# Performance work log

Hardware: AMD Instinct MI355X
Metric: run time of the kernel (lower is better)

The kernel has to match this reference:

```python
import jax, jax.numpy as jnp
import numpy as np
from jax import lax

NX, NY = 6, 6
NB = NX * NY            # 36 blocks
B, S = 64, 256          # batch, sample_count
EPS = 1e-6

def build_edges(nx, ny):
    edges = []
    for i in range(nx):
        for j in range(ny):
            for dx, dy in [(-1, 0), (0, -1), (0, 1), (1, 0)]:
                x, y = i + dx, j + dy
                if 0 <= x < nx and 0 <= y < ny:
                    edges.append((j * nx + i, y * nx + x))
    return np.array(edges, np.int32)   # (120, 2)

EDGES_NP = build_edges(NX, NY)
NE = len(EDGES_NP)  # 120

def setup_inputs() -> dict:
    key = jax.random.key(0)
    ks = jax.random.split(key, 24)
    f32 = jnp.float32
    d = {
        "image":      jax.random.normal(ks[0], (B, 1, 32, 32), f32),
        "edge_noise": jax.random.uniform(ks[1], (B, S, NE), f32),
        "u_s":        jax.random.uniform(ks[2], (B, S, NB), f32),
        "u_d":        jax.random.uniform(ks[3], (B, S, NB), f32),
        # CNN params (OIHW)
        "cw1": jax.random.normal(ks[4], (32, 1, 5, 5), f32) * 0.05,
        "cb1": jnp.zeros((32,), f32),
        "cw2": jax.random.normal(ks[5], (32, 32, 5, 5), f32) * 0.05,
        "cb2": jnp.zeros((32,), f32),
        "cw3": jax.random.normal(ks[6], (64, 32, 5, 5), f32) * 0.05,
        "cb3": jnp.zeros((64,), f32),
        "cw4": jax.random.normal(ks[7], (64, 64, 5, 5), f32) * 0.05,
        "cb4": jnp.zeros((64,), f32),
        # is_connected MLP
        "wc1": jax.random.normal(ks[8], (256, 256), f32) * 0.05,
        "bc1": jnp.zeros((256,), f32),
        "wc2": jax.random.normal(ks[9], (256, NE), f32) * 0.05,
        "bc2": jnp.zeros((NE,), f32),
        # is_endpoint MLP
        "we1": jax.random.normal(ks[10], (256, 256), f32) * 0.05,
        "be1": jnp.zeros((256,), f32),
        "we2": jax.random.normal(ks[11], (256, NB), f32) * 0.05,
        "be2": jnp.zeros((NB,), f32),
        "edges": jnp.asarray(EDGES_NP),  # (NE, 2) int32, constants
    }
    return d

def _conv(x, w, b):
    y = lax.conv_general_dilated(x, w, (1, 1), 'VALID',
                                 dimension_numbers=('NCHW', 'OIHW', 'NCHW'))
    return y + b[None, :, None, None]

def _pool2(x):
    return lax.reduce_window(x, -jnp.inf, lax.max, (1, 1, 2, 2), (1, 1, 2, 2), 'VALID')

def reference(image, edge_noise, u_s, u_d,
              cw1, cb1, cw2, cb2, cw3, cb3, cw4, cb4,
              wc1, bc1, wc2, bc2, we1, be1, we2, be2, edges):
    # ---- CNN feature extractor ----
    h = _conv(image, cw1, cb1)
    h = _conv(h, cw2, cb2)
    h = _pool2(h)
    h = _conv(h, cw3, cb3)
    h = _conv(h, cw4, cb4)
    h = _pool2(h)
    emb = h.reshape(h.shape[0], -1)              # (B, 256)

    # ---- heads ----
    p_conn = jax.nn.sigmoid(jax.nn.relu(emb @ wc1 + bc1) @ wc2 + bc2)   # (B, NE)
    p_ep   = jax.nn.sigmoid(jax.nn.relu(emb @ we1 + be1) @ we2 + be2)   # (B, NB)

    pc = jnp.clip(p_conn, EPS, 1.0 - EPS)
    pe = jnp.clip(p_ep, EPS, 1.0 - EPS)
    cat = pe / pe.sum(-1, keepdims=True)
    logcat = jnp.log(cat)                        # (B, NB)

    # ---- Monte-Carlo sampling (ISED blackbox) ----
    conn = (edge_noise < pc[:, None, :]).astype(pc.dtype)               # (B,S,NE) Bernoulli
    g_s = -jnp.log(-jnp.log(jnp.clip(u_s, EPS, 1.0 - EPS)))
    g_d = -jnp.log(-jnp.log(jnp.clip(u_d, EPS, 1.0 - EPS)))
    s_idx = jnp.argmax(logcat[:, None, :] + g_s, axis=-1)               # (B,S) categorical
    d_idx = jnp.argmax(logcat[:, None, :] + g_d, axis=-1)               # (B,S)

    # ---- batched BFS reachability via boolean matrix squaring ----
    oh_u = jax.nn.one_hot(edges[:, 0], NB, dtype=pc.dtype)              # (NE, NB)
    oh_v = jax.nn.one_hot(edges[:, 1], NB, dtype=pc.dtype)
    e_sym = jnp.einsum('eu,ev->euv', oh_u, oh_v) + jnp.einsum('eu,ev->evu', oh_u, oh_v)
    A = jnp.minimum(jnp.einsum('bse,euv->bsuv', conn, e_sym), 1.0)      # (B,S,36,36)

    R = jnp.minimum(A + jnp.eye(NB, dtype=A.dtype), 1.0)
    for _ in range(6):                           # (I+A)^(2^6), covers path len<=36
        R = jnp.minimum(R @ R, 1.0)
    P = jnp.minimum(A @ R, 1.0)                  # paths of length >= 1 (BFS semantics)

    Pv = jnp.take_along_axis(P, s_idx[:, :, None, None], axis=2)[:, :, 0, :]  # (B,S,36)
    exists = (jnp.take_along_axis(Pv, d_idx[:, :, None], axis=2)[:, :, 0] > 0.5).astype(pc.dtype)  # (B,S)

    # ---- sample-probability weighting (differentiable ISED estimator) ----
    logw = (conn * jnp.log(pc)[:, None, :] + (1.0 - conn) * jnp.log1p(-pc)[:, None, :]).sum(-1)
    logw = logw + jnp.take_along_axis(logcat, s_idx, axis=1) \
                + jnp.take_along_axis(logcat, d_idx, axis=1)            # (B,S)
    w = jax.nn.softmax(logw, axis=1)
    p1 = (w * exists).sum(axis=1)                # P(path exists)
    return jnp.stack([1.0 - p1, p1], axis=-1)    # (B, 2)
```

## Files before the change

### kernel.cpp

```cpp
#include <hip/hip_runtime.h>

typedef unsigned long long u64;
#define EPSF 1e-6f

__global__ __launch_bounds__(512) void k_conv1(const float* __restrict__ img,
                                               const float* __restrict__ cw1,
                                               const float* __restrict__ cb1,
                                               float* __restrict__ c1) {
  int slab = blockIdx.x, b = blockIdx.y;
  __shared__ float simg[32 * 33];
  for (int k = threadIdx.x; k < 1024; k += 512) {
    int y = k >> 5, x = k & 31;
    simg[y * 33 + x] = img[b * 1024 + k];
  }
  int half = threadIdx.x >> 8;
  int u = threadIdx.x & 255;
  int ocl = u >> 5;
  int x = u & 31;
  int oc = slab * 8 + ocl;
  int y0 = half * 14;
  float w[25];
#pragma unroll
  for (int k = 0; k < 25; ++k) w[k] = cw1[oc * 25 + k];
  float bias = cb1[oc];
  __syncthreads();
  if (x < 28) {
    float acc[5];
#pragma unroll
    for (int k = 0; k < 5; ++k) acc[k] = bias;
    float* outp = c1 + (b * 32 + oc) * 784 + x;
#pragma unroll
    for (int rr = 0; rr < 18; ++rr) {
      int r = y0 + rr;
      float in[5];
#pragma unroll
      for (int c = 0; c < 5; ++c) in[c] = simg[r * 33 + x + c];
#pragma unroll
      for (int ky = 0; ky < 5; ++ky) {
        if (rr < ky || rr - ky > 13) continue;
        int slot = (rr - ky) % 5;
#pragma unroll
        for (int kx = 0; kx < 5; ++kx)
          acc[slot] = fmaf(w[ky * 5 + kx], in[kx], acc[slot]);
      }
      if (rr >= 4) {
        int slot = (rr - 4) % 5;
        outp[(y0 + rr - 4) * 28] = acc[slot];
        acc[slot] = bias;
      }
    }
  }
}

__global__ __launch_bounds__(1024) void k_conv2(const float* __restrict__ c1,
                                                const float* __restrict__ cw2,
                                                const float* __restrict__ cb2,
                                                float* __restrict__ p1w) {
  int ocq = blockIdx.x, b = blockIdx.y;
  __shared__ float smem[32384];
  float* w2s = smem + 25984;
  int t = threadIdx.x;
  {
    const float4* src = (const float4*)(cw2 + ocq * 8 * 800);
    for (int k4 = t; k4 < 1600; k4 += 1024) {
      float4 v = src[k4];
      float vv[4] = {v.x, v.y, v.z, v.w};
      int k = k4 * 4;
#pragma unroll
      for (int r = 0; r < 4; ++r) {
        int kk = k + r;
        int o = kk / 800, rest = kk % 800;
        w2s[rest * 8 + o] = vv[r];
      }
    }
  }
  if (t < 784) {
    int row = t / 28, col = t % 28;
    int lofs = row * 29 + col;
    const float* src = c1 + (size_t)b * 25088 + t;
#pragma unroll
    for (int ic = 0; ic < 32; ++ic) smem[ic * 812 + lofs] = src[ic * 784];
  }
  int w = __builtin_amdgcn_readfirstlane(t >> 6);
  int opair = w & 3;
  int icq = w >> 2;
  int l = t & 63;
  int py = l >> 3, px = l & 7;
  int oc0 = ocq * 8 + opair * 2;
  float acc[2][9];
#pragma unroll
  for (int j = 0; j < 2; ++j)
#pragma unroll
    for (int e = 0; e < 9; ++e) acc[j][e] = 0.f;
  __syncthreads();

  const float* base0 = smem + icq * 8 * 812 + (3 * py) * 29 + 3 * px;
  const float* wbase = w2s + (size_t)icq * 8 * 200 + opair * 2;
#pragma unroll
  for (int ic = 0; ic < 8; ++ic) {
    float wa[25], wb[25];
#pragma unroll
    for (int k = 0; k < 25; ++k) {
      float2 wv = *(const float2*)(wbase + (ic * 25 + k) * 8);
      wa[k] = wv.x; wb[k] = wv.y;
    }
    const float* base = base0 + ic * 812;
#pragma unroll
    for (int rr = 0; rr < 7; ++rr) {
      float win[7];
#pragma unroll
      for (int m = 0; m < 7; ++m) win[m] = base[rr * 29 + m];
#pragma unroll
      for (int i = 0; i < 3; ++i) {
        if (i > rr || rr - i > 4) continue;
        int ky = rr - i;
#pragma unroll
        for (int kx = 0; kx < 5; ++kx) {
#pragma unroll
          for (int jj = 0; jj < 3; ++jj) {
            acc[0][i * 3 + jj] = fmaf(wa[ky * 5 + kx], win[jj + kx], acc[0][i * 3 + jj]);
            acc[1][i * 3 + jj] = fmaf(wb[ky * 5 + kx], win[jj + kx], acc[1][i * 3 + jj]);
          }
        }
      }
    }
  }

  __syncthreads();
  float* slots = smem;
  float* cbuf = smem + 9216;
  int chunk = opair * 2 * 576 + l * 9;
  if (icq >= 2) {
    float* d = slots + (icq - 2) * 4608 + chunk;
#pragma unroll
    for (int j = 0; j < 2; ++j)
#pragma unroll
      for (int e = 0; e < 9; ++e) d[j * 576 + e] = acc[j][e];
  }
  __syncthreads();
  if (icq < 2) {
    const float* s = slots + icq * 4608 + chunk;
#pragma unroll
    for (int j = 0; j < 2; ++j)
#pragma unroll
      for (int e = 0; e < 9; ++e) acc[j][e] += s[j * 576 + e];
  }
  __syncthreads();
  if (icq == 1) {
    float* d = slots + chunk;
#pragma unroll
    for (int j = 0; j < 2; ++j)
#pragma unroll
      for (int e = 0; e < 9; ++e) d[j * 576 + e] = acc[j][e];
  }
  __syncthreads();
  if (icq == 0) {
    const float* s = slots + chunk;
#pragma unroll
    for (int j = 0; j < 2; ++j) {
      float bias = cb2[oc0 + j];
#pragma unroll
      for (int i = 0; i < 3; ++i)
#pragma unroll
        for (int jj = 0; jj < 3; ++jj)
          cbuf[(opair * 2 + j) * 576 + (3 * py + i) * 24 + 3 * px + jj] =
              acc[j][i * 3 + jj] + s[j * 576 + i * 3 + jj] + bias;
    }
  }
  __syncthreads();
  for (int k = t; k < 1152; k += 1024) {
    int o = k / 144, rem = k % 144;
    int PY = rem / 12, PX = rem % 12;
    const float* b0 = cbuf + o * 576 + (2 * PY) * 24 + 2 * PX;
    float m = fmaxf(fmaxf(b0[0], b0[1]), fmaxf(b0[24], b0[25]));
    p1w[((size_t)b * 32 + ocq * 8 + o) * 144 + PY * 12 + PX] = m;
  }
}

__global__ __launch_bounds__(256) void k_conv3(const float* __restrict__ p1w,
                                               const float* __restrict__ cw3,
                                               const float* __restrict__ cb3,
                                               float* __restrict__ c3) {
  int oc8 = blockIdx.x, b = blockIdx.y;
  __shared__ float smem[11008];
  float* w3s = smem;
  float* ins = smem + 6400;
  int t = threadIdx.x;
  {
    const float4* src = (const float4*)(p1w + b * 32 * 144);
    float4* dst = (float4*)ins;
    for (int k = t; k < 1152; k += 256) dst[k] = src[k];
  }
  {
    const float4* src = (const float4*)(cw3 + oc8 * 8 * 800);
    for (int k4 = t; k4 < 1600; k4 += 256) {
      float4 v = src[k4];
      float vv[4] = {v.x, v.y, v.z, v.w};
      int k = k4 * 4;
#pragma unroll
      for (int r = 0; r < 4; ++r) {
        int kk = k + r;
        int o = kk / 800, rest = kk % 800;
        w3s[rest * 8 + o] = vv[r];
      }
    }
  }
  int g = t >> 4, p = t & 15;
  int ocg = p >> 3, row = p & 7;
  float acc[4][8];
#pragma unroll
  for (int j = 0; j < 4; ++j)
#pragma unroll
    for (int c = 0; c < 8; ++c) acc[j][c] = 0.f;
  __syncthreads();
#pragma unroll
  for (int icl = 0; icl < 2; ++icl) {
    int ic = g + icl * 16;
#pragma unroll
    for (int ky = 0; ky < 5; ++ky) {
      const float4* rp = (const float4*)(ins + ic * 144 + (row + ky) * 12);
      float win[12];
#pragma unroll
      for (int q = 0; q < 3; ++q) {
        float4 v = rp[q];
        win[4 * q] = v.x; win[4 * q + 1] = v.y; win[4 * q + 2] = v.z; win[4 * q + 3] = v.w;
      }
      const float* wb = w3s + (ic * 25 + ky * 5) * 8 + ocg * 4;
#pragma unroll
      for (int kx = 0; kx < 5; ++kx) {
        float wq[4];
        *(float4*)wq = *(const float4*)(wb + kx * 8);
#pragma unroll
        for (int c = 0; c < 8; ++c) {
#pragma unroll
          for (int j = 0; j < 4; ++j) acc[j][c] = fmaf(wq[j], win[c + kx], acc[j][c]);
        }
      }
    }
  }
  float* buf = smem;
  __syncthreads();
  if (g >= 8) {
    float* d = buf + (g - 8) * 512 + p * 32;
#pragma unroll
    for (int j = 0; j < 4; ++j)
#pragma unroll
      for (int c = 0; c < 8; ++c) d[j * 8 + c] = acc[j][c];
  }
  __syncthreads();
  if (g < 8) {
    const float* s = buf + g * 512 + p * 32;
#pragma unroll
    for (int j = 0; j < 4; ++j)
#pragma unroll
      for (int c = 0; c < 8; ++c) acc[j][c] += s[j * 8 + c];
  }
  __syncthreads();
  if (g >= 4 && g < 8) {
    float* d = buf + (g - 4) * 512 + p * 32;
#pragma unroll
    for (int j = 0; j < 4; ++j)
#pragma unroll
      for (int c = 0; c < 8; ++c) d[j * 8 + c] = acc[j][c];
  }
  __syncthreads();
  if (g < 4) {
    const float* s = buf + g * 512 + p * 32;
#pragma unroll
    for (int j = 0; j < 4; ++j)
#pragma unroll
      for (int c = 0; c < 8; ++c) acc[j][c] += s[j * 8 + c];
  }
  __syncthreads();
  if (g == 2 || g == 3) {
    float* d = buf + (g - 2) * 512 + p * 32;
#pragma unroll
    for (int j = 0; j < 4; ++j)
#pragma unroll
      for (int c = 0; c < 8; ++c) d[j * 8 + c] = acc[j][c];
  }
  __syncthreads();
  if (g < 2) {
    const float* s = buf + g * 512 + p * 32;
#pragma unroll
    for (int j = 0; j < 4; ++j)
#pragma unroll
      for (int c = 0; c < 8; ++c) acc[j][c] += s[j * 8 + c];
  }
  __syncthreads();
  if (g == 1) {
    float* d = buf + p * 32;
#pragma unroll
    for (int j = 0; j < 4; ++j)
#pragma unroll
      for (int c = 0; c < 8; ++c) d[j * 8 + c] = acc[j][c];
  }
  __syncthreads();
  if (g == 0) {
    const float* s = buf + p * 32;
#pragma unroll
    for (int j = 0; j < 4; ++j) {
      float bias = cb3[oc8 * 8 + ocg * 4 + j];
      float4 v0, v1;
      v0.x = acc[j][0] + s[j * 8 + 0] + bias; v0.y = acc[j][1] + s[j * 8 + 1] + bias;
      v0.z = acc[j][2] + s[j * 8 + 2] + bias; v0.w = acc[j][3] + s[j * 8 + 3] + bias;
      v1.x = acc[j][4] + s[j * 8 + 4] + bias; v1.y = acc[j][5] + s[j * 8 + 5] + bias;
      v1.z = acc[j][6] + s[j * 8 + 6] + bias; v1.w = acc[j][7] + s[j * 8 + 7] + bias;
      float* op = c3 + (b * 64 + oc8 * 8 + ocg * 4 + j) * 64 + row * 8;
      *(float4*)op = v0; *(float4*)(op + 4) = v1;
    }
  }
}

__global__ __launch_bounds__(256) void k_conv4(const float* __restrict__ c3,
                                               const float* __restrict__ cw4,
                                               const float* __restrict__ cb4,
                                               float* __restrict__ emb) {
  int oc8 = blockIdx.x, b = blockIdx.y;
  __shared__ float smem[17152];
  float* w4s = smem;
  float* ins = smem + 12800;
  int t = threadIdx.x;
  {
    const float4* src = (const float4*)(c3 + b * 4096);
    for (int k = t; k < 1024; k += 256) {
      int ic = k >> 4, q = k & 15;
      *(float4*)(ins + ic * 68 + q * 4) = src[k];
    }
  }
  {
    const float4* src = (const float4*)(cw4 + oc8 * 8 * 1600);
    for (int k4 = t; k4 < 3200; k4 += 256) {
      float4 v = src[k4];
      float vv[4] = {v.x, v.y, v.z, v.w};
      int k = k4 * 4;
#pragma unroll
      for (int r = 0; r < 4; ++r) {
        int kk = k + r;
        int o = kk / 1600, rest = kk % 1600;
        w4s[rest * 8 + o] = vv[r];
      }
    }
  }
  int g = t >> 3, p = t & 7;
  int ocg = p >> 2, row = p & 3;
  float acc[4][4];
#pragma unroll
  for (int j = 0; j < 4; ++j)
#pragma unroll
    for (int c = 0; c < 4; ++c) acc[j][c] = 0.f;
  __syncthreads();
#pragma unroll
  for (int icl = 0; icl < 2; ++icl) {
    int ic = g + icl * 32;
#pragma unroll
    for (int ky = 0; ky < 5; ++ky) {
      const float4* rp = (const float4*)(ins + ic * 68 + (row + ky) * 8);
      float win[8];
#pragma unroll
      for (int q = 0; q < 2; ++q) {
        float4 v = rp[q];
        win[4 * q] = v.x; win[4 * q + 1] = v.y; win[4 * q + 2] = v.z; win[4 * q + 3] = v.w;
      }
      const float* wb = w4s + (ic * 25 + ky * 5) * 8 + ocg * 4;
#pragma unroll
      for (int kx = 0; kx < 5; ++kx) {
        float wq[4];
        *(float4*)wq = *(const float4*)(wb + kx * 8);
#pragma unroll
        for (int c = 0; c < 4; ++c) {
#pragma unroll
          for (int j = 0; j < 4; ++j) acc[j][c] = fmaf(wq[j], win[c + kx], acc[j][c]);
        }
      }
    }
  }
  float* buf = smem;
#pragma unroll
  for (int half = 16; half >= 1; half >>= 1) {
    __syncthreads();
    if (g >= half && g < 2 * half) {
      float* d = buf + (g - half) * 128 + p * 16;
#pragma unroll
      for (int j = 0; j < 4; ++j)
#pragma unroll
        for (int c = 0; c < 4; ++c) d[j * 4 + c] = acc[j][c];
    }
    __syncthreads();
    if (g < half) {
      const float* s = buf + g * 128 + p * 16;
#pragma unroll
      for (int j = 0; j < 4; ++j)
#pragma unroll
        for (int c = 0; c < 4; ++c) acc[j][c] += s[j * 4 + c];
    }
  }
  float* pb = buf + 2048;
  if (g == 0) {
#pragma unroll
    for (int j = 0; j < 4; ++j) {
      float bias = cb4[oc8 * 8 + ocg * 4 + j];
#pragma unroll
      for (int c = 0; c < 4; ++c) pb[(ocg * 4 + j) * 16 + row * 4 + c] = acc[j][c] + bias;
    }
  }
  __syncthreads();
  if (t < 32) {
    int o = t >> 2, q = t & 3, py = q >> 1, px = q & 1;
    const float* b0 = pb + o * 16 + (2 * py) * 4 + 2 * px;
    float m = fmaxf(fmaxf(b0[0], b0[1]), fmaxf(b0[4], b0[5]));
    emb[b * 256 + (oc8 * 8 + o) * 4 + py * 2 + px] = m;
  }
}

__global__ __launch_bounds__(256) void k_heads(const float* __restrict__ emb,
    const float* __restrict__ wc1, const float* __restrict__ bc1,
    const float* __restrict__ wc2, const float* __restrict__ bc2,
    const float* __restrict__ we1, const float* __restrict__ be1,
    const float* __restrict__ we2, const float* __restrict__ be2,
    float* __restrict__ pcw, float* __restrict__ lpcw,
    float* __restrict__ l1mw, float* __restrict__ lcatw) {
  int head = blockIdx.x, b = blockIdx.y;
  int t = threadIdx.x;
  __shared__ float e_s[256], h_s[256];
  __shared__ float aux;
  e_s[t] = emb[b * 256 + t];
  __syncthreads();
  const float* W1 = head ? we1 : wc1;
  const float* B1 = head ? be1 : bc1;
  float s = B1[t];
  for (int i = 0; i < 256; i += 4) {
    s = fmaf(e_s[i], W1[i * 256 + t], s);
    s = fmaf(e_s[i + 1], W1[(i + 1) * 256 + t], s);
    s = fmaf(e_s[i + 2], W1[(i + 2) * 256 + t], s);
    s = fmaf(e_s[i + 3], W1[(i + 3) * 256 + t], s);
  }
  h_s[t] = fmaxf(s, 0.f);
  __syncthreads();
  int NO = head ? 36 : 120;
  const float* W2 = head ? we2 : wc2;
  const float* B2 = head ? be2 : bc2;
  if (t < NO) {
    float s2 = B2[t];
    for (int i = 0; i < 256; ++i) s2 = fmaf(h_s[i], W2[i * NO + t], s2);
    float p = 1.f / (1.f + expf(-s2));
    p = fminf(fmaxf(p, EPSF), 1.f - EPSF);
    if (head == 0) {
      pcw[b * 120 + t] = p;
      lpcw[b * 120 + t] = logf(p);
      l1mw[b * 120 + t] = log1pf(-p);
    } else {
      e_s[t] = p;
    }
  }
  if (head == 1) {
    __syncthreads();
    if (t == 0) {
      float sm = 0.f;
      for (int j2 = 0; j2 < 36; ++j2) sm += e_s[j2];
      aux = sm;
    }
    __syncthreads();
    if (t < 36) lcatw[b * 36 + t] = logf(e_s[t] / aux);
  }
}

__global__ __launch_bounds__(64) void k_mc1(const float* __restrict__ enoise,
    const float* __restrict__ us, const float* __restrict__ ud,
    const int* __restrict__ edges,
    const float* __restrict__ pcw, const float* __restrict__ lpcw,
    const float* __restrict__ l1mw, const float* __restrict__ lcatw,
    float* __restrict__ lw, float* __restrict__ exx) {
  int chunk = blockIdx.x, b = blockIdx.y, t = threadIdx.x;
  int s = chunk * 64 + t;
  __shared__ __align__(16) float pc_s[120];
  __shared__ __align__(16) float lpc_s[120];
  __shared__ __align__(16) float l1m_s[120];
  __shared__ __align__(16) float lcat_s[36];
  __shared__ __align__(16) int einfo[120];
  for (int k = t; k < 120; k += 64) {
    pc_s[k] = pcw[b * 120 + k];
    lpc_s[k] = lpcw[b * 120 + k];
    l1m_s[k] = l1mw[b * 120 + k];
    int u = edges[2 * k], v = edges[2 * k + 1];
    int d = v - u;
    int isV = (d == 6 || d == -6) ? 1 : 0;
    int pos = d > 0 ? u : v;
    einfo[k] = pos | (isV << 6);
  }
  if (t < 36) lcat_s[t] = lcatw[b * 36 + t];
  __syncthreads();

  float logw = 0.f;
  u64 H = 0, V = 0;
  {
    const float4* np = (const float4*)(enoise + ((size_t)(b * 256 + s)) * 120);
#pragma unroll
    for (int q = 0; q < 30; ++q) {
      float4 nz = np[q];
      float4 p4 = ((const float4*)pc_s)[q];
      float4 lp4 = ((const float4*)lpc_s)[q];
      float4 lm4 = ((const float4*)l1m_s)[q];
      int4 e4 = ((const int4*)einfo)[q];
      float nv[4] = {nz.x, nz.y, nz.z, nz.w};
      float pv[4] = {p4.x, p4.y, p4.z, p4.w};
      float lv[4] = {lp4.x, lp4.y, lp4.z, lp4.w};
      float mv[4] = {lm4.x, lm4.y, lm4.z, lm4.w};
      int ev[4] = {e4.x, e4.y, e4.z, e4.w};
#pragma unroll
      for (int r = 0; r < 4; ++r) {
        bool conn = nv[r] < pv[r];
        logw += conn ? lv[r] : mv[r];
        if (conn) {
          u64 bit = 1ull << (ev[r] & 63);
          if (ev[r] & 64) V |= bit; else H |= bit;
        }
      }
    }
  }
  int si = 0, di = 0;
  {
    const float4* up = (const float4*)(us + ((size_t)(b * 256 + s)) * 36);
    float best = -1e30f;
#pragma unroll
    for (int q = 0; q < 9; ++q) {
      float4 uv = up[q];
      float4 lc4 = ((const float4*)lcat_s)[q];
      float vv[4] = {uv.x, uv.y, uv.z, uv.w};
      float lc[4] = {lc4.x, lc4.y, lc4.z, lc4.w};
#pragma unroll
      for (int r = 0; r < 4; ++r) {
        float u = fminf(fmaxf(vv[r], EPSF), 1.f - EPSF);
        float gq = -logf(-logf(u));
        float val = lc[r] + gq;
        if (val > best) { best = val; si = q * 4 + r; }
      }
    }
  }
  {
    const float4* up = (const float4*)(ud + ((size_t)(b * 256 + s)) * 36);
    float best = -1e30f;
#pragma unroll
    for (int q = 0; q < 9; ++q) {
      float4 uv = up[q];
      float4 lc4 = ((const float4*)lcat_s)[q];
      float vv[4] = {uv.x, uv.y, uv.z, uv.w};
      float lc[4] = {lc4.x, lc4.y, lc4.z, lc4.w};
#pragma unroll
      for (int r = 0; r < 4; ++r) {
        float u = fminf(fmaxf(vv[r], EPSF), 1.f - EPSF);
        float gq = -logf(-logf(u));
        float val = lc[r] + gq;
        if (val > best) { best = val; di = q * 4 + r; }
      }
    }
  }
  logw += lcat_s[si] + lcat_s[di];

  u64 comp = 1ull << si;
  while (true) {
    u64 prev = comp;
    comp |= ((comp & H) << 1) | ((comp >> 1) & H);
    comp |= ((comp & V) << 6) | ((comp >> 6) & V);
    if (comp == prev) break;
  }
  float ex;
  if (si == di) ex = (comp != (1ull << si)) ? 1.f : 0.f;
  else ex = ((comp >> di) & 1ull) ? 1.f : 0.f;

  lw[b * 256 + s] = logw;
  exx[b * 256 + s] = ex;
}

__global__ __launch_bounds__(256) void k_mc2(const float* __restrict__ lw,
                                             const float* __restrict__ exx,
                                             float* __restrict__ out) {
  int b = blockIdx.x, t = threadIdx.x;
  __shared__ float red_s[256];
  float logw = lw[b * 256 + t];
  float ex = exx[b * 256 + t];
  red_s[t] = logw; __syncthreads();
  for (int off = 128; off > 0; off >>= 1) {
    if (t < off) red_s[t] = fmaxf(red_s[t], red_s[t + off]);
    __syncthreads();
  }
  float m = red_s[0]; __syncthreads();
  float evx = expf(logw - m);
  red_s[t] = evx; __syncthreads();
  for (int off = 128; off > 0; off >>= 1) {
    if (t < off) red_s[t] += red_s[t + off];
    __syncthreads();
  }
  float den = red_s[0]; __syncthreads();
  red_s[t] = evx * ex; __syncthreads();
  for (int off = 128; off > 0; off >>= 1) {
    if (t < off) red_s[t] += red_s[t + off];
    __syncthreads();
  }
  if (t == 0) {
    float p1v = red_s[0] / den;
    out[b * 2] = 1.f - p1v;
    out[b * 2 + 1] = p1v;
  }
}

extern "C" void kernel_launch(void* const* d_in, const int* in_sizes, int n_in,
                              void* d_out, int out_size, void* d_ws, size_t ws_size,
                              hipStream_t stream) {
  const float* image = (const float*)d_in[0];
  const float* enoise = (const float*)d_in[1];
  const float* us = (const float*)d_in[2];
  const float* udn = (const float*)d_in[3];
  const float* cw1 = (const float*)d_in[4];
  const float* cb1 = (const float*)d_in[5];
  const float* cw2 = (const float*)d_in[6];
  const float* cb2 = (const float*)d_in[7];
  const float* cw3 = (const float*)d_in[8];
  const float* cb3 = (const float*)d_in[9];
  const float* cw4 = (const float*)d_in[10];
  const float* cb4 = (const float*)d_in[11];
  const float* wc1 = (const float*)d_in[12];
  const float* bc1 = (const float*)d_in[13];
  const float* wc2 = (const float*)d_in[14];
  const float* bc2 = (const float*)d_in[15];
  const float* we1 = (const float*)d_in[16];
  const float* be1 = (const float*)d_in[17];
  const float* we2 = (const float*)d_in[18];
  const float* be2 = (const float*)d_in[19];
  const int* edges = (const int*)d_in[20];

  float* ws = (float*)d_ws;
  float* c1 = ws;
  float* p1w = ws + 1605632;
  float* c3 = ws + 1900544;
  float* emb = ws + 2162688;
  float* pcw = ws + 2179072;
  float* lpcw = ws + 2186752;
  float* l1mw = ws + 2194432;
  float* lcatw = ws + 2202112;
  float* lw = ws + 2204416;
  float* exx = ws + 2220800;
  float* outp = (float*)d_out;

  k_conv1<<<dim3(4, 64), dim3(512), 0, stream>>>(image, cw1, cb1, c1);
  k_conv2<<<dim3(4, 64), dim3(1024), 0, stream>>>(c1, cw2, cb2, p1w);
  k_conv3<<<dim3(8, 64), dim3(256), 0, stream>>>(p1w, cw3, cb3, c3);
  k_conv4<<<dim3(8, 64), dim3(256), 0, stream>>>(c3, cw4, cb4, emb);
  k_heads<<<dim3(2, 64), dim3(256), 0, stream>>>(emb, wc1, bc1, wc2, bc2,
                                                 we1, be1, we2, be2,
                                                 pcw, lpcw, l1mw, lcatw);
  k_mc1<<<dim3(4, 64), dim3(64), 0, stream>>>(enoise, us, udn, edges,
                                              pcw, lpcw, l1mw, lcatw, lw, exx);
  k_mc2<<<dim3(64), dim3(256), 0, stream>>>(lw, exx, outp);
}
```

Measured before the change: 124.2 us.

## Regroup conv2 waves to four output channels each with an eight-way input-channel split

k_conv2 now has each wave compute four output channels over four input channels, instead of two output channels over eight. The full 7x7 input window is loaded into registers once per input channel and reused across the four channels through float4 weight loads, which cuts LDS reads per FMA. The cross-wave reduction gains an extra level (8→4→2→1), and launch_bounds adds a min-blocks hint. The trade-off is higher register pressure from 36 accumulators plus a 49-element window, and one more barrier-separated reduction stage.

Result: faster. 119.6 us (-3.7%).

```diff
diff --git a/kernel.cpp b/kernel.cpp
--- a/kernel.cpp
+++ b/kernel.cpp
@@ -52,10 +52,10 @@
   }
 }
 
-__global__ __launch_bounds__(1024) void k_conv2(const float* __restrict__ c1,
-                                                const float* __restrict__ cw2,
-                                                const float* __restrict__ cb2,
-                                                float* __restrict__ p1w) {
+__global__ __launch_bounds__(1024, 4) void k_conv2(const float* __restrict__ c1,
+                                                   const float* __restrict__ cw2,
+                                                   const float* __restrict__ cb2,
+                                                   float* __restrict__ p1w) {
   int ocq = blockIdx.x, b = blockIdx.y;
   __shared__ float smem[32384];
   float* w2s = smem + 25984;
@@ -82,44 +82,46 @@
     for (int ic = 0; ic < 32; ++ic) smem[ic * 812 + lofs] = src[ic * 784];
   }
   int w = __builtin_amdgcn_readfirstlane(t >> 6);
-  int opair = w & 3;
-  int icq = w >> 2;
+  int ocg = w & 1;
+  int icq = w >> 1;
   int l = t & 63;
   int py = l >> 3, px = l & 7;
-  int oc0 = ocq * 8 + opair * 2;
-  float acc[2][9];
-#pragma unroll
-  for (int j = 0; j < 2; ++j)
-#pragma unroll
-    for (int e = 0; e < 9; ++e) acc[j][e] = 0.f;
-  __syncthreads();
-
-  const float* base0 = smem + icq * 8 * 812 + (3 * py) * 29 + 3 * px;
-  const float* wbase = w2s + (size_t)icq * 8 * 200 + opair * 2;
-#pragma unroll
-  for (int ic = 0; ic < 8; ++ic) {
-    float wa[25], wb[25];
-#pragma unroll
-    for (int k = 0; k < 25; ++k) {
-      float2 wv = *(const float2*)(wbase + (ic * 25 + k) * 8);
-      wa[k] = wv.x; wb[k] = wv.y;
-    }
-    const float* base = base0 + ic * 812;
-#pragma unroll
-    for (int rr = 0; rr < 7; ++rr) {
-      float win[7];
-#pragma unroll
-      for (int m = 0; m < 7; ++m) win[m] = base[rr * 29 + m];
+  int oc0 = ocq * 8 + ocg * 4;
+  float acc[4][9];
+#pragma unroll
+  for (int o = 0; o < 4; ++o)
+#pragma unroll
+    for (int e = 0; e < 9; ++e) acc[o][e] = 0.f;
+  __syncthreads();
+
+  const float* base0 = smem + icq * 4 * 812 + (3 * py) * 29 + 3 * px;
+  const float* wk0 = w2s + icq * 800 + ocg * 4;
+#pragma unroll
+  for (int icl = 0; icl < 4; ++icl) {
+    const float* base = base0 + icl * 812;
+    float win[7][7];
+#pragma unroll
+    for (int rr = 0; rr < 7; ++rr)
+#pragma unroll
+      for (int m = 0; m < 7; ++m) win[rr][m] = base[rr * 29 + m];
+    const float* wk = wk0 + icl * 200;
+#pragma unroll
+    for (int ky = 0; ky < 5; ++ky) {
+      float wq[5][4];
+#pragma unroll
+      for (int kx = 0; kx < 5; ++kx)
+        *(float4*)wq[kx] = *(const float4*)(wk + (ky * 5 + kx) * 8);
 #pragma unroll
       for (int i = 0; i < 3; ++i) {
-        if (i > rr || rr - i > 4) continue;
-        int ky = rr - i;
 #pragma unroll
         for (int kx = 0; kx < 5; ++kx) {
 #pragma unroll
           for (int jj = 0; jj < 3; ++jj) {
-            acc[0][i * 3 + jj] = fmaf(wa[ky * 5 + kx], win[jj + kx], acc[0][i * 3 + jj]);
-            acc[1][i * 3 + jj] = fmaf(wb[ky * 5 + kx], win[jj + kx], acc[1][i * 3 + jj]);
+            float v = win[i + ky][jj + kx];
+            acc[0][i * 3 + jj] = fmaf(wq[kx][0], v, acc[0][i * 3 + jj]);
+            acc[1][i * 3 + jj] = fmaf(wq[kx][1], v, acc[1][i * 3 + jj]);
+            acc[2][i * 3 + jj] = fmaf(wq[kx][2], v, acc[2][i * 3 + jj]);
+            acc[3][i * 3 + jj] = fmaf(wq[kx][3], v, acc[3][i * 3 + jj]);
           }
         }
       }
@@ -128,43 +130,59 @@
 
   __syncthreads();
   float* slots = smem;
-  float* cbuf = smem + 9216;
-  int chunk = opair * 2 * 576 + l * 9;
-  if (icq >= 2) {
+  float* cbuf = smem + 18432;
+  int chunk = ocg * 2304 + l * 9;
+  if (icq >= 4) {
+    float* d = slots + (icq - 4) * 4608 + chunk;
+#pragma unroll
+    for (int o = 0; o < 4; ++o)
+#pragma unroll
+      for (int e = 0; e < 9; ++e) d[o * 576 + e] = acc[o][e];
+  }
+  __syncthreads();
+  if (icq < 4) {
+    const float* s = slots + icq * 4608 + chunk;
+#pragma unroll
+    for (int o = 0; o < 4; ++o)
+#pragma unroll
+      for (int e = 0; e < 9; ++e) acc[o][e] += s[o * 576 + e];
+  }
+  __syncthreads();
+  if (icq == 2 || icq == 3) {
     float* d = slots + (icq - 2) * 4608 + chunk;
 #pragma unroll
-    for (int j = 0; j < 2; ++j)
-#pragma unroll
-      for (int e = 0; e < 9; ++e) d[j * 576 + e] = acc[j][e];
+    for (int o = 0; o < 4; ++o)
+#pragma unroll
+      for (int e = 0; e < 9; ++e) d[o * 576 + e] = acc[o][e];
   }
   __syncthreads();
   if (icq < 2) {
     const float* s = slots + icq * 4608 + chunk;
 #pragma unroll
-    for (int j = 0; j < 2; ++j)
-#pragma unroll
-      for (int e = 0; e < 9; ++e) acc[j][e] += s[j * 576 + e];
+    for (int o = 0; o < 4; ++o)
+#pragma unroll
+      for (int e = 0; e < 9; ++e) acc[o][e] += s[o * 576 + e];
   }
   __syncthreads();
   if (icq == 1) {
     float* d = slots + chunk;
 #pragma unroll
-    for (int j = 0; j < 2; ++j)
-#pragma unroll
-      for (int e = 0; e < 9; ++e) d[j * 576 + e] = acc[j][e];
+    for (int o = 0; o < 4; ++o)
+#pragma unroll
+      for (int e = 0; e < 9; ++e) d[o * 576 + e] = acc[o][e];
   }
   __syncthreads();
   if (icq == 0) {
     const float* s = slots + chunk;
 #pragma unroll
-    for (int j = 0; j < 2; ++j) {
-      float bias = cb2[oc0 + j];
+    for (int o = 0; o < 4; ++o) {
+      float bias = cb2[oc0 + o];
 #pragma unroll
       for (int i = 0; i < 3; ++i)
 #pragma unroll
         for (int jj = 0; jj < 3; ++jj)
-          cbuf[(opair * 2 + j) * 576 + (3 * py + i) * 24 + 3 * px + jj] =
-              acc[j][i * 3 + jj] + s[j * 576 + i * 3 + jj] + bias;
+          cbuf[(ocg * 4 + o) * 576 + (3 * py + i) * 24 + 3 * px + jj] =
+              acc[o][i * 3 + jj] + s[o * 576 + i * 3 + jj] + bias;
     }
   }
   __syncthreads();
```
